# Kernel tuning notes

Hardware: AMD Instinct MI355X
Metric: run time of the kernel (lower is better)

The kernel has to match this reference:

```python
import jax, jax.numpy as jnp
import numpy as np

N_USER = 50000
N_ITEM = 50000
N_EDGE = 1600000
D_IN = 64
D_OUT = 64


def _mean_agg(msgs, dst, num_dst):
    # copy_u + mean: segment-mean of edge messages onto dst nodes; zero for
    # zero-in-degree nodes (DGL default).
    s = jax.ops.segment_sum(msgs, dst, num_segments=num_dst)          # [Nd, D]
    cnt = jax.ops.segment_sum(jnp.ones((msgs.shape[0],), msgs.dtype), dst,
                              num_segments=num_dst)                    # [Nd]
    return s / jnp.maximum(cnt, 1.0)[:, None]


def setup_inputs() -> dict:
    key = jax.random.key(0)
    ks = jax.random.split(key, 12)
    return {
        'user_feat': jax.random.normal(ks[0], (N_USER, D_IN), jnp.float32),
        'item_feat': jax.random.normal(ks[1], (N_ITEM, D_IN), jnp.float32),
        'rate_src': jax.random.randint(ks[2], (N_EDGE,), 0, N_USER, jnp.int64 if jax.config.jax_enable_x64 else jnp.int32),
        'rate_dst': jax.random.randint(ks[3], (N_EDGE,), 0, N_ITEM, jnp.int64 if jax.config.jax_enable_x64 else jnp.int32),
        'rev_src': jax.random.randint(ks[4], (N_EDGE,), 0, N_ITEM, jnp.int64 if jax.config.jax_enable_x64 else jnp.int32),
        'rev_dst': jax.random.randint(ks[5], (N_EDGE,), 0, N_USER, jnp.int64 if jax.config.jax_enable_x64 else jnp.int32),
        'W_rate': jax.random.normal(ks[6], (D_IN, D_OUT), jnp.float32) * (1.0 / np.sqrt(D_IN)),
        'b_rate': jnp.zeros((D_OUT,), jnp.float32),
        'W_rev': jax.random.normal(ks[7], (D_IN, D_OUT), jnp.float32) * (1.0 / np.sqrt(D_IN)),
        'b_rev': jnp.zeros((D_OUT,), jnp.float32),
        'loop_weight': jax.random.normal(ks[8], (D_IN, D_OUT), jnp.float32) * (1.0 / np.sqrt(D_IN)),
        'h_bias': jnp.zeros((D_OUT,), jnp.float32),
    }


def reference(user_feat, item_feat, rate_src, rate_dst, rev_src, rev_dst,
              W_rate, b_rate, W_rev, b_rev, loop_weight, h_bias):
    # Per-etype Linear on source-node features (applied node-wise, as in torch).
    Wh_rate = user_feat @ W_rate + b_rate      # [Nu, Dout], etype 'rate': user->item
    Wh_rev = item_feat @ W_rev + b_rev         # [Ni, Dout], etype 'rated-by': item->user

    # copy_u + mean per etype, cross-reduce 'sum' (one etype per dst ntype here).
    h_item = _mean_agg(Wh_rate[rate_src], rate_dst, N_ITEM)
    h_user = _mean_agg(Wh_rev[rev_src], rev_dst, N_USER)

    # self-loop + bias (dropout p=0.0 is identity)
    h_user = h_user + user_feat @ loop_weight + h_bias
    h_item = h_item + item_feat @ loop_weight + h_bias
    return (h_user, h_item)
```

## Files before the change

### kernel.cpp

```cpp
#include <hip/hip_runtime.h>

#define N_USER 50000
#define N_ITEM 50000
#define N_NODE 50000
#define N_EDGE 1600000
#define D 64

#define CB_SHIFT 8
#define NBKT 196
#define BCAP 10240
#define CHUNK 8192
#define NCH ((N_EDGE + CHUNK - 1) / CHUNK)
#define NCAST 3125

typedef __attribute__((ext_vector_type(8))) short short8;
typedef __attribute__((ext_vector_type(4))) float floatx4;

__device__ __forceinline__ unsigned short f32_to_bf16(float x) {
    unsigned u = __float_as_uint(x);
    unsigned r = (u + 0x7FFFu + ((u >> 16) & 1u)) >> 16;
    return (unsigned short)r;
}
__device__ __forceinline__ float bf16_to_f32(unsigned short h) {
    return __uint_as_float(((unsigned)h) << 16);
}

__device__ __forceinline__ void acc2(float* a, int k, unsigned u) {
    a[k]     += __uint_as_float(u << 16);
    a[k + 1] += __uint_as_float(u & 0xFFFF0000u);
}
__device__ __forceinline__ void acc8(float* a, uint4 w) {
    acc2(a, 0, w.x); acc2(a, 2, w.y); acc2(a, 4, w.z); acc2(a, 6, w.w);
}

__global__ __launch_bounds__(256) void cast_bin(
    const float4* __restrict__ fU, ushort4* __restrict__ bU,
    const float4* __restrict__ fI, ushort4* __restrict__ bI,
    const int* __restrict__ srcA, const int* __restrict__ dstA, unsigned* __restrict__ gbinA,
    const int* __restrict__ srcB, const int* __restrict__ dstB, unsigned* __restrict__ gbinB,
    int* __restrict__ fcur)
{
    __shared__ unsigned lbin[CHUNK];
    __shared__ int hist[NBKT];
    __shared__ int lofs[NBKT];
    __shared__ int lcur[NBKT];
    __shared__ int gbase[NBKT];
    __shared__ int sc[256];

    const int id = blockIdx.x;

    if (id >= 2 * NCH) {
        const int cid = id - 2 * NCH;
        const int et = (cid >= NCAST) ? 1 : 0;
        const float4* __restrict__ in = et ? fI : fU;
        ushort4* __restrict__ out     = et ? bI : bU;
        int i = (cid - et * NCAST) * 256 + threadIdx.x;
        float4 v = in[i];
        ushort4 o;
        o.x = f32_to_bf16(v.x); o.y = f32_to_bf16(v.y);
        o.z = f32_to_bf16(v.z); o.w = f32_to_bf16(v.w);
        out[i] = o;
        return;
    }

    const int et = (id >= NCH) ? 1 : 0;
    const int chunk = id - et * NCH;
    const int* __restrict__ src = et ? srcB : srcA;
    const int* __restrict__ dst = et ? dstB : dstA;
    unsigned* __restrict__ gbin = et ? gbinB : gbinA;
    int* __restrict__ fc = fcur + et * NBKT;

    const int base = chunk * CHUNK;
    const int nE = min(CHUNK, N_EDGE - base);
    const int n4 = nE >> 2;
    const int4* dst4 = (const int4*)(dst + base);
    const int4* src4 = (const int4*)(src + base);
    const int tid = threadIdx.x;

    for (int i = tid; i < NBKT; i += 256) hist[i] = 0;
    __syncthreads();

    for (int i = tid; i < n4; i += 256) {
        int4 d = dst4[i];
        atomicAdd(&hist[d.x >> CB_SHIFT], 1);
        atomicAdd(&hist[d.y >> CB_SHIFT], 1);
        atomicAdd(&hist[d.z >> CB_SHIFT], 1);
        atomicAdd(&hist[d.w >> CB_SHIFT], 1);
    }
    __syncthreads();

    int v = (tid < NBKT) ? hist[tid] : 0;
    sc[tid] = v;
    __syncthreads();
    for (int o = 1; o < 256; o <<= 1) {
        int t = (tid >= o) ? sc[tid - o] : 0;
        __syncthreads();
        sc[tid] += t;
        __syncthreads();
    }
    if (tid < NBKT) {
        int excl = sc[tid] - v;
        lofs[tid] = excl;
        lcur[tid] = excl;
        gbase[tid] = v ? (tid * BCAP + atomicAdd(&fc[tid], v)) : 0;
    }
    __syncthreads();

    for (int i = tid; i < n4; i += 256) {
        int4 d = dst4[i];
        int4 s = src4[i];
        { int p = atomicAdd(&lcur[d.x >> CB_SHIFT], 1); lbin[p] = ((unsigned)d.x << 16) | (unsigned)s.x; }
        { int p = atomicAdd(&lcur[d.y >> CB_SHIFT], 1); lbin[p] = ((unsigned)d.y << 16) | (unsigned)s.y; }
        { int p = atomicAdd(&lcur[d.z >> CB_SHIFT], 1); lbin[p] = ((unsigned)d.z << 16) | (unsigned)s.z; }
        { int p = atomicAdd(&lcur[d.w >> CB_SHIFT], 1); lbin[p] = ((unsigned)d.w << 16) | (unsigned)s.w; }
    }
    __syncthreads();

    const int wv = tid >> 6, ln = tid & 63;
    for (int b = wv; b < NBKT; b += 4) {
        const int s0 = lofs[b], c = hist[b], g = gbase[b];
        for (int t = ln; t < c; t += 64) gbin[g + t] = lbin[s0 + t];
    }
}

__global__ __launch_bounds__(256) void bucket_sort(
    const unsigned* __restrict__ gbinI, unsigned short* __restrict__ srtI,
    int* __restrict__ offI, int* __restrict__ cntI,
    const unsigned* __restrict__ gbinU, unsigned short* __restrict__ srtU,
    int* __restrict__ offU, int* __restrict__ cntU,
    const int* __restrict__ fcur)
{
    const int et = blockIdx.y;
    const unsigned* __restrict__ gbin = et ? gbinU : gbinI;
    unsigned short* __restrict__ srt  = et ? srtU : srtI;
    int* __restrict__ off   = et ? offU : offI;
    int* __restrict__ cntG  = et ? cntU : cntI;
    const int b = blockIdx.x;
    const int startg = b * BCAP;
    const int n = fcur[et * NBKT + b];
    const int nodebase = b << CB_SHIFT;
    const int tid = threadIdx.x;

    __shared__ int cnt[256];
    __shared__ int sc[256];
    __shared__ int pos[256];
    __shared__ unsigned short lsrt[BCAP];

    cnt[tid] = 0;
    __syncthreads();

    for (int i = tid; i < n; i += 256)
        atomicAdd(&cnt[(int)(gbin[startg + i] >> 16) - nodebase], 1);
    __syncthreads();

    int v = cnt[tid];
    sc[tid] = v;
    __syncthreads();
    for (int o = 1; o < 256; o <<= 1) {
        int t = (tid >= o) ? sc[tid - o] : 0;
        __syncthreads();
        sc[tid] += t;
        __syncthreads();
    }
    {
        int excl = sc[tid] - v;
        pos[tid] = excl;
        int node = nodebase + tid;
        if (node < N_NODE) { off[node] = startg + excl; cntG[node] = v; }
    }
    __syncthreads();

    for (int i = tid; i < n; i += 256) {
        unsigned p = gbin[startg + i];
        int q = atomicAdd(&pos[(int)(p >> 16) - nodebase], 1);
        lsrt[q] = (unsigned short)(p & 0xFFFFu);
    }
    __syncthreads();

    for (int i = tid; i < n; i += 256) srt[startg + i] = lsrt[i];
}

__global__ __launch_bounds__(256) void aggregate_kernel(
    const uint4* __restrict__ itemB,
    const uint4* __restrict__ userB,
    const int* __restrict__ offU, const int* __restrict__ cntU, const unsigned short* __restrict__ srtU,
    const int* __restrict__ offI, const int* __restrict__ cntI, const unsigned short* __restrict__ srtI,
    uint4* __restrict__ aggU, uint4* __restrict__ aggI)
{
    int g = blockIdx.x * 32 + (threadIdx.x >> 3);
    if (g >= N_USER + N_ITEM) return;
    const int lane = threadIdx.x & 7;

    const bool isUser = (g < N_USER);
    const int d = isUser ? g : g - N_USER;
    const uint4* __restrict__ tab = isUser ? itemB : userB;
    const int* __restrict__ off     = isUser ? offU : offI;
    const int* __restrict__ cntG    = isUser ? cntU : cntI;
    const unsigned short* __restrict__ srt = isUser ? srtU : srtI;
    uint4* __restrict__ agg         = isUser ? aggU : aggI;

    const int start = off[d];
    const int c     = cntG[d];
    const int end   = start + c;

    float aA[8] = {0.f, 0.f, 0.f, 0.f, 0.f, 0.f, 0.f, 0.f};
    float aB[8] = {0.f, 0.f, 0.f, 0.f, 0.f, 0.f, 0.f, 0.f};

    int e = start;
    for (; e + 8 <= end; e += 8) {
        int s0 = (int)srt[e],     s1 = (int)srt[e + 1];
        int s2 = (int)srt[e + 2], s3 = (int)srt[e + 3];
        int s4 = (int)srt[e + 4], s5 = (int)srt[e + 5];
        int s6 = (int)srt[e + 6], s7 = (int)srt[e + 7];
        uint4 w0 = tab[(size_t)s0 * 8 + lane];
        uint4 w1 = tab[(size_t)s1 * 8 + lane];
        uint4 w2 = tab[(size_t)s2 * 8 + lane];
        uint4 w3 = tab[(size_t)s3 * 8 + lane];
        uint4 w4 = tab[(size_t)s4 * 8 + lane];
        uint4 w5 = tab[(size_t)s5 * 8 + lane];
        uint4 w6 = tab[(size_t)s6 * 8 + lane];
        uint4 w7 = tab[(size_t)s7 * 8 + lane];
        acc8(aA, w0); acc8(aB, w1); acc8(aA, w2); acc8(aB, w3);
        acc8(aA, w4); acc8(aB, w5); acc8(aA, w6); acc8(aB, w7);
    }
    for (; e + 4 <= end; e += 4) {
        int s0 = (int)srt[e],     s1 = (int)srt[e + 1];
        int s2 = (int)srt[e + 2], s3 = (int)srt[e + 3];
        uint4 w0 = tab[(size_t)s0 * 8 + lane];
        uint4 w1 = tab[(size_t)s1 * 8 + lane];
        uint4 w2 = tab[(size_t)s2 * 8 + lane];
        uint4 w3 = tab[(size_t)s3 * 8 + lane];
        acc8(aA, w0); acc8(aB, w1); acc8(aA, w2); acc8(aB, w3);
    }
    for (; e < end; ++e) {
        uint4 w = tab[(size_t)(int)srt[e] * 8 + lane];
        acc8(aA, w);
    }
    #pragma unroll
    for (int k = 0; k < 8; ++k) aA[k] += aB[k];

    const float inv = (c > 0) ? 1.0f / (float)c : 0.0f;
    uint4 o;
    o.x = (unsigned)f32_to_bf16(aA[0] * inv) | ((unsigned)f32_to_bf16(aA[1] * inv) << 16);
    o.y = (unsigned)f32_to_bf16(aA[2] * inv) | ((unsigned)f32_to_bf16(aA[3] * inv) << 16);
    o.z = (unsigned)f32_to_bf16(aA[4] * inv) | ((unsigned)f32_to_bf16(aA[5] * inv) << 16);
    o.w = (unsigned)f32_to_bf16(aA[6] * inv) | ((unsigned)f32_to_bf16(aA[7] * inv) << 16);
    agg[(size_t)d * 8 + lane] = o;
}

__global__ __launch_bounds__(256, 4) void final_gemm(
    const unsigned short* __restrict__ aggU_, const unsigned short* __restrict__ featU_,
    const int* __restrict__ cntU_, const float* __restrict__ WU,
    const float* __restrict__ beU,
    const unsigned short* __restrict__ aggI_, const unsigned short* __restrict__ featI_,
    const int* __restrict__ cntI_, const float* __restrict__ WI,
    const float* __restrict__ beI,
    const float* __restrict__ loop_w, const float* __restrict__ h_bias,
    float* __restrict__ out)
{
    const int et = blockIdx.y;
    const unsigned short* __restrict__ agg  = et ? aggI_ : aggU_;
    const unsigned short* __restrict__ feat = et ? featI_ : featU_;
    const int* __restrict__ cntG            = et ? cntI_ : cntU_;
    const float* __restrict__ W             = et ? WI : WU;
    const float* __restrict__ b_et          = et ? beI : beU;
    float* __restrict__ outN = out + (et ? (size_t)N_USER * D : 0);

    __shared__ unsigned short sWt[64][72];
    __shared__ unsigned short sLt[64][72];
    __shared__ float sbe[64], sbh[64];
    __shared__ int sCnt[64];

    const int tid = threadIdx.x;
    const int row0 = blockIdx.x * 64;

    for (int i = tid; i < 4096; i += 256) {
        int k = i >> 6, n = i & 63;
        sWt[n][k] = f32_to_bf16(W[i]);
        sLt[n][k] = f32_to_bf16(loop_w[i]);
    }
    if (tid < 64) {
        sbe[tid] = b_et[tid];
        sbh[tid] = h_bias[tid];
        int r = row0 + tid;
        sCnt[tid] = (r < N_NODE) ? cntG[r] : 0;
    }
    __syncthreads();

    const int wave = tid >> 6;
    const int lane = tid & 63;
    const int quad = lane >> 4;
    const int l16  = lane & 15;

    const int rowA = row0 + wave * 16 + l16;
    const int rA = (rowA < N_NODE) ? rowA : (N_NODE - 1);
    short8 aAgg0  = *(const short8*)(agg  + (size_t)rA * 64 +      quad * 8);
    short8 aAgg1  = *(const short8*)(agg  + (size_t)rA * 64 + 32 + quad * 8);
    short8 aFeat0 = *(const short8*)(feat + (size_t)rA * 64 +      quad * 8);
    short8 aFeat1 = *(const short8*)(feat + (size_t)rA * 64 + 32 + quad * 8);

    floatx4 acc[4];
    #pragma unroll
    for (int t = 0; t < 4; ++t) {
        const int n = t * 16 + l16;
        short8 bW0 = *(const short8*)&sWt[n][     quad * 8];
        short8 bW1 = *(const short8*)&sWt[n][32 + quad * 8];
        short8 bL0 = *(const short8*)&sLt[n][     quad * 8];
        short8 bL1 = *(const short8*)&sLt[n][32 + quad * 8];
        floatx4 a = {0.f, 0.f, 0.f, 0.f};
        a = __builtin_amdgcn_mfma_f32_16x16x32_bf16(aAgg0,  bW0, a, 0, 0, 0);
        a = __builtin_amdgcn_mfma_f32_16x16x32_bf16(aAgg1,  bW1, a, 0, 0, 0);
        a = __builtin_amdgcn_mfma_f32_16x16x32_bf16(aFeat0, bL0, a, 0, 0, 0);
        a = __builtin_amdgcn_mfma_f32_16x16x32_bf16(aFeat1, bL1, a, 0, 0, 0);
        acc[t] = a;
    }

    #pragma unroll
    for (int t = 0; t < 4; ++t) {
        const int col = t * 16 + l16;
        const float bh = sbh[col], be = sbe[col];
        #pragma unroll
        for (int i = 0; i < 4; ++i) {
            int lrow = wave * 16 + quad * 4 + i;
            int r = row0 + lrow;
            if (r < N_NODE) {
                float v = acc[t][i] + bh + (sCnt[lrow] > 0 ? be : 0.f);
                outN[(size_t)r * D + col] = v;
            }
        }
    }
}

extern "C" void kernel_launch(void* const* d_in, const int* in_sizes, int n_in,
                              void* d_out, int out_size, void* d_ws, size_t ws_size,
                              hipStream_t stream)
{
    const float* user_feat = (const float*)d_in[0];
    const float* item_feat = (const float*)d_in[1];
    const int*   rate_src  = (const int*)d_in[2];
    const int*   rate_dst  = (const int*)d_in[3];
    const int*   rev_src   = (const int*)d_in[4];
    const int*   rev_dst   = (const int*)d_in[5];
    const float* W_rate    = (const float*)d_in[6];
    const float* b_rate    = (const float*)d_in[7];
    const float* W_rev     = (const float*)d_in[8];
    const float* b_rev     = (const float*)d_in[9];
    const float* loop_w    = (const float*)d_in[10];
    const float* h_bias    = (const float*)d_in[11];
    float* out = (float*)d_out;

    char* p = (char*)d_ws;
    ushort4* userB = (ushort4*)p; p += (size_t)N_USER * D * 2;
    ushort4* itemB = (ushort4*)p; p += (size_t)N_ITEM * D * 2;
    unsigned* gbinI = (unsigned*)p; p += (size_t)NBKT * BCAP * 4;
    unsigned* gbinU = (unsigned*)p; p += (size_t)NBKT * BCAP * 4;
    unsigned short* srtI = (unsigned short*)p; p += (size_t)NBKT * BCAP * 2;
    unsigned short* srtU = (unsigned short*)p; p += (size_t)NBKT * BCAP * 2;
    ushort4* aggI  = (ushort4*)p; p += (size_t)N_NODE * D * 2;
    ushort4* aggU  = (ushort4*)p; p += (size_t)N_NODE * D * 2;
    int* offI = (int*)p; p += (size_t)N_NODE * 4;
    int* offU = (int*)p; p += (size_t)N_NODE * 4;
    int* cntI = (int*)p; p += (size_t)N_NODE * 4;
    int* cntU = (int*)p; p += (size_t)N_NODE * 4;
    int* fcur = (int*)p; p += (size_t)(2 * NBKT) * 4;
    (void)ws_size;

    hipMemsetAsync(fcur, 0, (size_t)(2 * NBKT) * sizeof(int), stream);

    cast_bin<<<dim3(2 * NCH + 2 * NCAST), 256, 0, stream>>>(
        (const float4*)user_feat, userB, (const float4*)item_feat, itemB,
        rate_src, rate_dst, gbinI,
        rev_src,  rev_dst,  gbinU, fcur);

    bucket_sort<<<dim3(NBKT, 2), 256, 0, stream>>>(
        gbinI, srtI, offI, cntI,
        gbinU, srtU, offU, cntU, fcur);

    aggregate_kernel<<<(N_USER + N_ITEM + 31) / 32, 256, 0, stream>>>(
        (const uint4*)itemB, (const uint4*)userB,
        offU, cntU, srtU,
        offI, cntI, srtI,
        (uint4*)aggU, (uint4*)aggI);

    final_gemm<<<dim3((N_NODE + 63) / 64, 2), 256, 0, stream>>>(
        (const unsigned short*)aggU, (const unsigned short*)userB, cntU, W_rev, b_rev,
        (const unsigned short*)aggI, (const unsigned short*)itemB, cntI, W_rate, b_rate,
        loop_w, h_bias, out);

    (void)in_sizes; (void)n_in; (void)out_size;
}
```

Baseline: 197.8 us.

## Split aggregation by feature half and edge type across interleaved blocks for L2 locality

```diff
diff --git a/kernel.cpp b/kernel.cpp
--- a/kernel.cpp
+++ b/kernel.cpp
@@ -12,6 +12,10 @@
 #define CHUNK 8192
 #define NCH ((N_EDGE + CHUNK - 1) / CHUNK)
 #define NCAST 3125
+
+#define AGG_NPB 64
+#define AGG_CPB ((N_NODE + AGG_NPB - 1) / AGG_NPB)
+#define AGG_GRID (AGG_CPB * 4)
 
 typedef __attribute__((ext_vector_type(8))) short short8;
 typedef __attribute__((ext_vector_type(4))) float floatx4;
@@ -187,21 +191,27 @@
     const int* __restrict__ offI, const int* __restrict__ cntI, const unsigned short* __restrict__ srtI,
     uint4* __restrict__ aggU, uint4* __restrict__ aggI)
 {
-    int g = blockIdx.x * 32 + (threadIdx.x >> 3);
-    if (g >= N_USER + N_ITEM) return;
-    const int lane = threadIdx.x & 7;
-
-    const bool isUser = (g < N_USER);
-    const int d = isUser ? g : g - N_USER;
-    const uint4* __restrict__ tab = isUser ? itemB : userB;
-    const int* __restrict__ off     = isUser ? offU : offI;
-    const int* __restrict__ cntG    = isUser ? cntU : cntI;
-    const unsigned short* __restrict__ srt = isUser ? srtU : srtI;
-    uint4* __restrict__ agg         = isUser ? aggU : aggI;
-
-    const int start = off[d];
-    const int c     = cntG[d];
+    const int b = blockIdx.x;
+    const int slot  = b & 7;
+    const int combo = slot >> 1;
+    const int et    = combo & 1;
+    const int dh    = combo >> 1;
+    const int chunk = (b >> 3) * 2 + (slot & 1);
+    const int tid = threadIdx.x;
+    const int node = chunk * AGG_NPB + (tid >> 2);
+    if (node >= N_NODE) return;
+    const int lane = tid & 3;
+
+    const uint4* __restrict__ tab = et ? userB : itemB;
+    const int* __restrict__ off   = et ? offI : offU;
+    const int* __restrict__ cntG  = et ? cntI : cntU;
+    const unsigned short* __restrict__ srt = et ? srtI : srtU;
+    uint4* __restrict__ agg       = et ? aggI : aggU;
+
+    const int start = off[node];
+    const int c     = cntG[node];
     const int end   = start + c;
+    const int rofs  = dh * 4 + lane;
 
     float aA[8] = {0.f, 0.f, 0.f, 0.f, 0.f, 0.f, 0.f, 0.f};
     float aB[8] = {0.f, 0.f, 0.f, 0.f, 0.f, 0.f, 0.f, 0.f};
@@ -212,28 +222,28 @@
         int s2 = (int)srt[e + 2], s3 = (int)srt[e + 3];
         int s4 = (int)srt[e + 4], s5 = (int)srt[e + 5];
         int s6 = (int)srt[e + 6], s7 = (int)srt[e + 7];
-        uint4 w0 = tab[(size_t)s0 * 8 + lane];
-        uint4 w1 = tab[(size_t)s1 * 8 + lane];
-        uint4 w2 = tab[(size_t)s2 * 8 + lane];
-        uint4 w3 = tab[(size_t)s3 * 8 + lane];
-        uint4 w4 = tab[(size_t)s4 * 8 + lane];
-        uint4 w5 = tab[(size_t)s5 * 8 + lane];
-        uint4 w6 = tab[(size_t)s6 * 8 + lane];
-        uint4 w7 = tab[(size_t)s7 * 8 + lane];
+        uint4 w0 = tab[(size_t)s0 * 8 + rofs];
+        uint4 w1 = tab[(size_t)s1 * 8 + rofs];
+        uint4 w2 = tab[(size_t)s2 * 8 + rofs];
+        uint4 w3 = tab[(size_t)s3 * 8 + rofs];
+        uint4 w4 = tab[(size_t)s4 * 8 + rofs];
+        uint4 w5 = tab[(size_t)s5 * 8 + rofs];
+        uint4 w6 = tab[(size_t)s6 * 8 + rofs];
+        uint4 w7 = tab[(size_t)s7 * 8 + rofs];
         acc8(aA, w0); acc8(aB, w1); acc8(aA, w2); acc8(aB, w3);
         acc8(aA, w4); acc8(aB, w5); acc8(aA, w6); acc8(aB, w7);
     }
     for (; e + 4 <= end; e += 4) {
         int s0 = (int)srt[e],     s1 = (int)srt[e + 1];
         int s2 = (int)srt[e + 2], s3 = (int)srt[e + 3];
-        uint4 w0 = tab[(size_t)s0 * 8 + lane];
-        uint4 w1 = tab[(size_t)s1 * 8 + lane];
-        uint4 w2 = tab[(size_t)s2 * 8 + lane];
-        uint4 w3 = tab[(size_t)s3 * 8 + lane];
+        uint4 w0 = tab[(size_t)s0 * 8 + rofs];
+        uint4 w1 = tab[(size_t)s1 * 8 + rofs];
+        uint4 w2 = tab[(size_t)s2 * 8 + rofs];
+        uint4 w3 = tab[(size_t)s3 * 8 + rofs];
         acc8(aA, w0); acc8(aB, w1); acc8(aA, w2); acc8(aB, w3);
     }
     for (; e < end; ++e) {
-        uint4 w = tab[(size_t)(int)srt[e] * 8 + lane];
+        uint4 w = tab[(size_t)(int)srt[e] * 8 + rofs];
         acc8(aA, w);
     }
     #pragma unroll
@@ -245,7 +255,7 @@
     o.y = (unsigned)f32_to_bf16(aA[2] * inv) | ((unsigned)f32_to_bf16(aA[3] * inv) << 16);
     o.z = (unsigned)f32_to_bf16(aA[4] * inv) | ((unsigned)f32_to_bf16(aA[5] * inv) << 16);
     o.w = (unsigned)f32_to_bf16(aA[6] * inv) | ((unsigned)f32_to_bf16(aA[7] * inv) << 16);
-    agg[(size_t)d * 8 + lane] = o;
+    agg[(size_t)node * 8 + rofs] = o;
 }
 
 __global__ __launch_bounds__(256, 4) void final_gemm(
@@ -376,7 +386,7 @@
         gbinI, srtI, offI, cntI,
         gbinU, srtU, offU, cntU, fcur);
 
-    aggregate_kernel<<<(N_USER + N_ITEM + 31) / 32, 256, 0, stream>>>(
+    aggregate_kernel<<<AGG_GRID, 256, 0, stream>>>(
         (const uint4*)itemB, (const uint4*)userB,
         offU, cntU, srtU,
         offI, cntI, srtI,
```

Measured after the change: 223.0 us. +12.7%, slower.

## Fuse neighbor aggregation with final MFMA GEMM, keeping aggregates in LDS

Applied to the files above, without the earlier changes.

```diff
diff --git a/kernel.cpp b/kernel.cpp
--- a/kernel.cpp
+++ b/kernel.cpp
@@ -12,6 +12,7 @@
 #define CHUNK 8192
 #define NCH ((N_EDGE + CHUNK - 1) / CHUNK)
 #define NCAST 3125
+#define NAGB ((N_NODE + 31) / 32)
 
 typedef __attribute__((ext_vector_type(8))) short short8;
 typedef __attribute__((ext_vector_type(4))) float floatx4;
@@ -21,8 +22,8 @@
     unsigned r = (u + 0x7FFFu + ((u >> 16) & 1u)) >> 16;
     return (unsigned short)r;
 }
-__device__ __forceinline__ float bf16_to_f32(unsigned short h) {
-    return __uint_as_float(((unsigned)h) << 16);
+__device__ __forceinline__ unsigned pack2(float lo, float hi) {
+    return (unsigned)f32_to_bf16(lo) | ((unsigned)f32_to_bf16(hi) << 16);
 }
 
 __device__ __forceinline__ void acc2(float* a, int k, unsigned u) {
@@ -180,28 +181,49 @@
     for (int i = tid; i < n; i += 256) srt[startg + i] = lsrt[i];
 }
 
-__global__ __launch_bounds__(256) void aggregate_kernel(
-    const uint4* __restrict__ itemB,
-    const uint4* __restrict__ userB,
+__global__ __launch_bounds__(256) void agg_gemm(
+    const uint4* __restrict__ userB, const uint4* __restrict__ itemB,
     const int* __restrict__ offU, const int* __restrict__ cntU, const unsigned short* __restrict__ srtU,
     const int* __restrict__ offI, const int* __restrict__ cntI, const unsigned short* __restrict__ srtI,
-    uint4* __restrict__ aggU, uint4* __restrict__ aggI)
+    const float* __restrict__ W_rev, const float* __restrict__ b_rev,
+    const float* __restrict__ W_rate, const float* __restrict__ b_rate,
+    const float* __restrict__ loop_w, const float* __restrict__ h_bias,
+    float* __restrict__ out)
 {
-    int g = blockIdx.x * 32 + (threadIdx.x >> 3);
-    if (g >= N_USER + N_ITEM) return;
-    const int lane = threadIdx.x & 7;
-
-    const bool isUser = (g < N_USER);
-    const int d = isUser ? g : g - N_USER;
-    const uint4* __restrict__ tab = isUser ? itemB : userB;
-    const int* __restrict__ off     = isUser ? offU : offI;
-    const int* __restrict__ cntG    = isUser ? cntU : cntI;
-    const unsigned short* __restrict__ srt = isUser ? srtU : srtI;
-    uint4* __restrict__ agg         = isUser ? aggU : aggI;
-
-    const int start = off[d];
-    const int c     = cntG[d];
-    const int end   = start + c;
+    const int et = blockIdx.y;
+    const uint4* __restrict__ tab = et ? userB : itemB;
+    const int* __restrict__ off   = et ? offI : offU;
+    const int* __restrict__ cntG  = et ? cntI : cntU;
+    const unsigned short* __restrict__ srt = et ? srtI : srtU;
+    const float* __restrict__ W    = et ? W_rate : W_rev;
+    const float* __restrict__ b_et = et ? b_rate : b_rev;
+    const unsigned short* __restrict__ feat =
+        (const unsigned short*)(et ? itemB : userB);
+    float* __restrict__ outN = out + (et ? (size_t)N_USER * D : 0);
+
+    __shared__ unsigned short sWt[64][72];
+    __shared__ unsigned short sLt[64][72];
+    __shared__ unsigned sA[32][33];
+    __shared__ float sbe[64], sbh[64];
+    __shared__ int sCnt[32];
+
+    const int tid = threadIdx.x;
+
+    for (int i = tid; i < 4096; i += 256) {
+        int k = i >> 6, n = i & 63;
+        sWt[n][k] = f32_to_bf16(W[i]);
+        sLt[n][k] = f32_to_bf16(loop_w[i]);
+    }
+    if (tid < 64) { sbe[tid] = b_et[tid]; sbh[tid] = h_bias[tid]; }
+
+    const int grp  = tid >> 3;
+    const int lane = tid & 7;
+    const int node = blockIdx.x * 32 + grp;
+    const bool valid = (node < N_NODE);
+    const int nd = valid ? node : (N_NODE - 1);
+    const int start = off[nd];
+    const int c = valid ? cntG[nd] : 0;
+    const int end = start + c;
 
     float aA[8] = {0.f, 0.f, 0.f, 0.f, 0.f, 0.f, 0.f, 0.f};
     float aB[8] = {0.f, 0.f, 0.f, 0.f, 0.f, 0.f, 0.f, 0.f};
@@ -240,69 +262,31 @@
     for (int k = 0; k < 8; ++k) aA[k] += aB[k];
 
     const float inv = (c > 0) ? 1.0f / (float)c : 0.0f;
-    uint4 o;
-    o.x = (unsigned)f32_to_bf16(aA[0] * inv) | ((unsigned)f32_to_bf16(aA[1] * inv) << 16);
-    o.y = (unsigned)f32_to_bf16(aA[2] * inv) | ((unsigned)f32_to_bf16(aA[3] * inv) << 16);
-    o.z = (unsigned)f32_to_bf16(aA[4] * inv) | ((unsigned)f32_to_bf16(aA[5] * inv) << 16);
-    o.w = (unsigned)f32_to_bf16(aA[6] * inv) | ((unsigned)f32_to_bf16(aA[7] * inv) << 16);
-    agg[(size_t)d * 8 + lane] = o;
-}
-
-__global__ __launch_bounds__(256, 4) void final_gemm(
-    const unsigned short* __restrict__ aggU_, const unsigned short* __restrict__ featU_,
-    const int* __restrict__ cntU_, const float* __restrict__ WU,
-    const float* __restrict__ beU,
-    const unsigned short* __restrict__ aggI_, const unsigned short* __restrict__ featI_,
-    const int* __restrict__ cntI_, const float* __restrict__ WI,
-    const float* __restrict__ beI,
-    const float* __restrict__ loop_w, const float* __restrict__ h_bias,
-    float* __restrict__ out)
-{
-    const int et = blockIdx.y;
-    const unsigned short* __restrict__ agg  = et ? aggI_ : aggU_;
-    const unsigned short* __restrict__ feat = et ? featI_ : featU_;
-    const int* __restrict__ cntG            = et ? cntI_ : cntU_;
-    const float* __restrict__ W             = et ? WI : WU;
-    const float* __restrict__ b_et          = et ? beI : beU;
-    float* __restrict__ outN = out + (et ? (size_t)N_USER * D : 0);
-
-    __shared__ unsigned short sWt[64][72];
-    __shared__ unsigned short sLt[64][72];
-    __shared__ float sbe[64], sbh[64];
-    __shared__ int sCnt[64];
-
-    const int tid = threadIdx.x;
-    const int row0 = blockIdx.x * 64;
-
-    for (int i = tid; i < 4096; i += 256) {
-        int k = i >> 6, n = i & 63;
-        sWt[n][k] = f32_to_bf16(W[i]);
-        sLt[n][k] = f32_to_bf16(loop_w[i]);
-    }
-    if (tid < 64) {
-        sbe[tid] = b_et[tid];
-        sbh[tid] = h_bias[tid];
-        int r = row0 + tid;
-        sCnt[tid] = (r < N_NODE) ? cntG[r] : 0;
-    }
+    sA[grp][lane * 4 + 0] = pack2(aA[0] * inv, aA[1] * inv);
+    sA[grp][lane * 4 + 1] = pack2(aA[2] * inv, aA[3] * inv);
+    sA[grp][lane * 4 + 2] = pack2(aA[4] * inv, aA[5] * inv);
+    sA[grp][lane * 4 + 3] = pack2(aA[6] * inv, aA[7] * inv);
+    if (lane == 0) sCnt[grp] = c;
     __syncthreads();
 
     const int wave = tid >> 6;
-    const int lane = tid & 63;
-    const int quad = lane >> 4;
-    const int l16  = lane & 15;
-
-    const int rowA = row0 + wave * 16 + l16;
-    const int rA = (rowA < N_NODE) ? rowA : (N_NODE - 1);
-    short8 aAgg0  = *(const short8*)(agg  + (size_t)rA * 64 +      quad * 8);
-    short8 aAgg1  = *(const short8*)(agg  + (size_t)rA * 64 + 32 + quad * 8);
-    short8 aFeat0 = *(const short8*)(feat + (size_t)rA * 64 +      quad * 8);
-    short8 aFeat1 = *(const short8*)(feat + (size_t)rA * 64 + 32 + quad * 8);
-
-    floatx4 acc[4];
+    const int l    = tid & 63;
+    const int quad = l >> 4;
+    const int l16  = l & 15;
+    const int rowbase = (wave & 1) * 16;
+    const int colbase = (wave >> 1) * 32;
+
+    const int lrow = rowbase + l16;
+    short8 aAgg0 = *(const short8*)&sA[lrow][     quad * 4];
+    short8 aAgg1 = *(const short8*)&sA[lrow][16 + quad * 4];
+    const int grow = blockIdx.x * 32 + lrow;
+    const int gr = (grow < N_NODE) ? grow : (N_NODE - 1);
+    short8 aFeat0 = *(const short8*)(feat + (size_t)gr * 64 +      quad * 8);
+    short8 aFeat1 = *(const short8*)(feat + (size_t)gr * 64 + 32 + quad * 8);
+
     #pragma unroll
-    for (int t = 0; t < 4; ++t) {
-        const int n = t * 16 + l16;
+    for (int t = 0; t < 2; ++t) {
+        const int n = colbase + t * 16 + l16;
         short8 bW0 = *(const short8*)&sWt[n][     quad * 8];
         short8 bW1 = *(const short8*)&sWt[n][32 + quad * 8];
         short8 bL0 = *(const short8*)&sLt[n][     quad * 8];
@@ -312,20 +296,13 @@
         a = __builtin_amdgcn_mfma_f32_16x16x32_bf16(aAgg1,  bW1, a, 0, 0, 0);
         a = __builtin_amdgcn_mfma_f32_16x16x32_bf16(aFeat0, bL0, a, 0, 0, 0);
         a = __builtin_amdgcn_mfma_f32_16x16x32_bf16(aFeat1, bL1, a, 0, 0, 0);
-        acc[t] = a;
-    }
-
-    #pragma unroll
-    for (int t = 0; t < 4; ++t) {
-        const int col = t * 16 + l16;
-        const float bh = sbh[col], be = sbe[col];
+        const float bh = sbh[n], be = sbe[n];
         #pragma unroll
         for (int i = 0; i < 4; ++i) {
-            int lrow = wave * 16 + quad * 4 + i;
-            int r = row0 + lrow;
+            const int rl = rowbase + quad * 4 + i;
+            const int r = blockIdx.x * 32 + rl;
             if (r < N_NODE) {
-                float v = acc[t][i] + bh + (sCnt[lrow] > 0 ? be : 0.f);
-                outN[(size_t)r * D + col] = v;
+                outN[(size_t)r * D + n] = a[i] + bh + (sCnt[rl] > 0 ? be : 0.f);
             }
         }
     }
@@ -356,8 +333,6 @@
     unsigned* gbinU = (unsigned*)p; p += (size_t)NBKT * BCAP * 4;
     unsigned short* srtI = (unsigned short*)p; p += (size_t)NBKT * BCAP * 2;
     unsigned short* srtU = (unsigned short*)p; p += (size_t)NBKT * BCAP * 2;
-    ushort4* aggI  = (ushort4*)p; p += (size_t)N_NODE * D * 2;
-    ushort4* aggU  = (ushort4*)p; p += (size_t)N_NODE * D * 2;
     int* offI = (int*)p; p += (size_t)N_NODE * 4;
     int* offU = (int*)p; p += (size_t)N_NODE * 4;
     int* cntI = (int*)p; p += (size_t)N_NODE * 4;
@@ -376,15 +351,11 @@
         gbinI, srtI, offI, cntI,
         gbinU, srtU, offU, cntU, fcur);
 
-    aggregate_kernel<<<(N_USER + N_ITEM + 31) / 32, 256, 0, stream>>>(
-        (const uint4*)itemB, (const uint4*)userB,
+    agg_gemm<<<dim3(NAGB, 2), 256, 0, stream>>>(
+        (const uint4*)userB, (const uint4*)itemB,
         offU, cntU, srtU,
         offI, cntI, srtI,
-        (uint4*)aggU, (uint4*)aggI);
-
-    final_gemm<<<dim3((N_NODE + 63) / 64, 2), 256, 0, stream>>>(
-        (const unsigned short*)aggU, (const unsigned short*)userB, cntU, W_rev, b_rev,
-        (const unsigned short*)aggI, (const unsigned short*)itemB, cntI, W_rate, b_rate,
+        W_rev, b_rev, W_rate, b_rate,
         loop_w, h_bias, out);
 
     (void)in_sizes; (void)n_in; (void)out_size;
```

Result: slower. 202.8 us (+2.5%).
